# Performance work log

Hardware: AMD Instinct MI355X
Metric: run time of the kernel (lower is better)

The kernel has to match this reference:

```python
import jax, jax.numpy as jnp
import numpy as np
import math

B, T, C, H = 16384, 64, 48, 48


def setup_inputs() -> dict:
    key = jax.random.key(0)
    kx, kq, kk, kv = jax.random.split(key, 4)
    return {
        "x": jax.random.normal(kx, (B, T, C), dtype=jnp.float32),
        "Wq": jax.random.normal(kq, (C, H), dtype=jnp.float32) * 0.02,
        "Wk": jax.random.normal(kk, (C, H), dtype=jnp.float32) * 0.02,
        "Wv": jax.random.normal(kv, (C, H), dtype=jnp.float32) * 0.02,
    }


def reference(x, Wq, Wk, Wv):
    # x: [B, T, C]; projections (Linear with bias=False): [B, T, H]
    q = x @ Wq
    k = x @ Wk
    v = x @ Wv
    scale = 1.0 / math.sqrt(H)
    # scores: [B, T, T]
    wei = jnp.einsum("bth,bsh->bts", q, k) * scale
    causal = jnp.tril(jnp.ones((T, T), dtype=bool))  # tril mask, T==BLOCK_SIZE
    wei = jnp.where(causal, wei, -jnp.inf)
    wei = jax.nn.softmax(wei, axis=-1)
    # dropout is identity in eval mode
    return jnp.einsum("bts,bsh->bth", wei, v)
```

## Files before the change

kernel.cpp:

```cpp
#include <hip/hip_runtime.h>
#include <math.h>

typedef __bf16 bf16x8 __attribute__((ext_vector_type(8)));
typedef float f32x4 __attribute__((ext_vector_type(4)));
typedef unsigned short u16;

__device__ __forceinline__ u16 f2b(float f) {
  unsigned u = __builtin_bit_cast(unsigned, f);
  u = (u + 0x7fffu + ((u >> 16) & 1u)) >> 16;
  return (u16)u;
}

__device__ __forceinline__ f32x4 mfma16(bf16x8 a, bf16x8 b, f32x4 c) {
  return __builtin_amdgcn_mfma_f32_16x16x32_bf16(a, b, c, 0, 0, 0);
}

__device__ __forceinline__ int sw(int r, int c) {
  return (r << 6) + ((((c >> 3) ^ r) & 7) << 3) + (c & 7);
}
__device__ __forceinline__ int swc(int r, int ch) {
  return (r << 6) + (((ch ^ r) & 7) << 3);
}

__global__ __launch_bounds__(256) void head_prep(const float* __restrict__ Wq,
                                                 const float* __restrict__ Wk,
                                                 const float* __restrict__ Wv,
                                                 u16* __restrict__ ws) {
  __shared__ float wq[2304], wk[2304], wv[2304];
  const float scale = 0.14433756729740643f;
  for (int i = threadIdx.x; i < 2304; i += 256) {
    wq[i] = Wq[i];
    wk[i] = Wk[i];
    wv[i] = Wv[i];
  }
  __syncthreads();
  for (int idx = threadIdx.x; idx < 96 * 64; idx += 256) {
    int r = idx >> 6, c = idx & 63;
    float v = 0.f;
    if (c < 48) {
      if (r < 48) {
        float a = 0.f;
        for (int h = 0; h < 48; ++h) a += wq[c * 48 + h] * wk[r * 48 + h];
        v = a * scale;
      } else {
        v = wv[c * 48 + (r - 48)];
      }
    }
    ws[sw(r, c)] = f2b(v);
  }
}

__global__ __launch_bounds__(256, 6) void head_main(const float* __restrict__ x,
                                                    const u16* __restrict__ wimg,
                                                    float* __restrict__ out) {
  __shared__ u16 lds[208 * 64];
  u16* const R0 = lds;
  u16* const X  = lds + 96 * 64;
  u16* const VT = lds + 160 * 64;

  const int tid  = threadIdx.x;
  const int lane = tid & 63;
  const int w    = tid >> 6;
  const int qd   = lane >> 4;
  const int col  = lane & 15;
  const long b   = blockIdx.x;

  {
    const uint4* src = (const uint4*)wimg;
    uint4* dst = (uint4*)lds;
    dst[tid]       = src[tid];
    dst[tid + 256] = src[tid + 256];
    dst[tid + 512] = src[tid + 512];
  }
  {
    const float* xb = x + b * 3072;
#pragma unroll
    for (int it = 0; it < 3; ++it) {
      int flat = tid * 4 + it * 1024;
      float4 v = *(const float4*)(xb + flat);
      int row = flat / 48;
      int c0  = flat % 48;
      ushort4 pk;
      pk.x = f2b(v.x); pk.y = f2b(v.y); pk.z = f2b(v.z); pk.w = f2b(v.w);
      *(ushort4*)(X + sw(row, c0)) = pk;
    }
    int zr = tid >> 2;
    int zq = tid & 3;
    ushort4 z = {0, 0, 0, 0};
    *(ushort4*)(X + swc(zr, 6 + (zq >> 1)) + (zq & 1) * 4) = z;
  }
  __syncthreads();

  f32x4 aq[3];
  {
    const int ar = 16 * w + col;
    const bf16x8 xa0 = *(const bf16x8*)(X + swc(ar, qd));
    const bf16x8 xa1 = *(const bf16x8*)(X + swc(ar, qd + 4));
    const u16* WM = R0;
    const u16* WV = R0 + 48 * 64;
#pragma unroll
    for (int n = 0; n < 3; ++n) {
      const int br = 16 * n + col;
      const int b0 = swc(br, qd);
      const int b1 = swc(br, qd + 4);
      f32x4 av = {0.f, 0.f, 0.f, 0.f};
      av = mfma16(xa0, *(const bf16x8*)(WV + b0), av);
      av = mfma16(xa1, *(const bf16x8*)(WV + b1), av);
      f32x4 a = {0.f, 0.f, 0.f, 0.f};
      a = mfma16(xa0, *(const bf16x8*)(WM + b0), a);
      a = mfma16(xa1, *(const bf16x8*)(WM + b1), a);
      aq[n] = a;
      ushort4 pv;
      pv.x = f2b(av[0]); pv.y = f2b(av[1]); pv.z = f2b(av[2]); pv.w = f2b(av[3]);
      *(ushort4*)(VT + sw(16 * n + col, 16 * w + qd * 4)) = pv;
    }
  }
  __syncthreads();

#pragma unroll
  for (int n = 0; n < 3; ++n)
#pragma unroll
    for (int i = 0; i < 4; ++i)
      R0[sw(16 * w + qd * 4 + i, 16 * n + col)] = f2b(aq[n][i]);
  __threadfence_block();

  float sv[4][4];
  {
    const int ar = 16 * w + col;
    const bf16x8 qa0 = *(const bf16x8*)(R0 + swc(ar, qd));
    const bf16x8 qa1 = *(const bf16x8*)(R0 + swc(ar, qd + 4));
#pragma unroll
    for (int st = 0; st < 4; ++st) {
      const int br = 16 * st + col;
      f32x4 a = {0.f, 0.f, 0.f, 0.f};
      a = mfma16(qa0, *(const bf16x8*)(X + swc(br, qd)), a);
      a = mfma16(qa1, *(const bf16x8*)(X + swc(br, qd + 4)), a);
#pragma unroll
      for (int i = 0; i < 4; ++i) sv[st][i] = a[i];
    }
  }

  float m4[4] = {-INFINITY, -INFINITY, -INFINITY, -INFINITY};
#pragma unroll
  for (int st = 0; st < 4; ++st)
#pragma unroll
    for (int i = 0; i < 4; ++i) {
      int tg = 16 * w + qd * 4 + i;
      int sg = 16 * st + col;
      float v = (sg <= tg) ? sv[st][i] : -INFINITY;
      sv[st][i] = v;
      m4[i] = fmaxf(m4[i], v);
    }
#pragma unroll
  for (int d = 1; d < 16; d <<= 1)
#pragma unroll
    for (int i = 0; i < 4; ++i) m4[i] = fmaxf(m4[i], __shfl_xor(m4[i], d, 64));
  float l4[4] = {0.f, 0.f, 0.f, 0.f};
#pragma unroll
  for (int st = 0; st < 4; ++st)
#pragma unroll
    for (int i = 0; i < 4; ++i) {
      float p = __expf(sv[st][i] - m4[i]);
      sv[st][i] = p;
      l4[i] += p;
    }
#pragma unroll
  for (int d = 1; d < 16; d <<= 1)
#pragma unroll
    for (int i = 0; i < 4; ++i) l4[i] += __shfl_xor(l4[i], d, 64);

  __syncthreads();

#pragma unroll
  for (int st = 0; st < 4; ++st)
#pragma unroll
    for (int i = 0; i < 4; ++i)
      X[sw(16 * w + qd * 4 + i, 16 * st + col)] = f2b(sv[st][i]);
  __threadfence_block();

  f32x4 o0 = {0.f, 0.f, 0.f, 0.f}, o1 = o0, o2 = o0;
  {
    const int pr = 16 * w + col;
#pragma unroll
    for (int kt = 0; kt < 2; ++kt) {
      const int ch = qd + 4 * kt;
      bf16x8 pa = *(const bf16x8*)(X + swc(pr, ch));
      o0 = mfma16(pa, *(const bf16x8*)(VT + swc(0  + col, ch)), o0);
      o1 = mfma16(pa, *(const bf16x8*)(VT + swc(16 + col, ch)), o1);
      o2 = mfma16(pa, *(const bf16x8*)(VT + swc(32 + col, ch)), o2);
    }
  }
  float rl[4];
#pragma unroll
  for (int i = 0; i < 4; ++i) rl[i] = __builtin_amdgcn_rcpf(l4[i]);

  float* ob = out + b * 3072 + (16 * w + qd * 4) * 48 + col;
#pragma unroll
  for (int i = 0; i < 4; ++i) {
    ob[i * 48 +  0] = o0[i] * rl[i];
    ob[i * 48 + 16] = o1[i] * rl[i];
    ob[i * 48 + 32] = o2[i] * rl[i];
  }
}

extern "C" void kernel_launch(void* const* d_in, const int* in_sizes, int n_in,
                              void* d_out, int out_size, void* d_ws, size_t ws_size,
                              hipStream_t stream) {
  const float* x  = (const float*)d_in[0];
  const float* Wq = (const float*)d_in[1];
  const float* Wk = (const float*)d_in[2];
  const float* Wv = (const float*)d_in[3];
  u16* wimg = (u16*)d_ws;
  head_prep<<<1, 256, 0, stream>>>(Wq, Wk, Wv, wimg);
  head_main<<<16384, 256, 0, stream>>>(x, wimg, (float*)d_out);
}
```

Baseline: 343.1 us.

## Read weights from global, transpose score MFMAs, and cut LDS footprint and barriers

The main kernel no longer copies the 24 KB weight image into LDS. It now reads the weight fragments directly from global memory, where they should hit in cache, and stores the weight image unswizzled. The Q and score MFMAs swap their operands, so each lane holds one query row's scores, and each softmax reduction needs only two cross-lane shuffles instead of four. The P tile reuses the Q buffer, which removes one __syncthreads and shrinks LDS from 26 KB to 22 KB, so more blocks can fit per CU. Each wave loads only its own 16 rows of x. The cost is global-latency loads for the weights on every block and an extra shuffle to spread the reciprocals.

```diff
diff --git a/kernel.cpp b/kernel.cpp
--- a/kernel.cpp
+++ b/kernel.cpp
@@ -46,17 +46,17 @@
         v = wv[c * 48 + (r - 48)];
       }
     }
-    ws[sw(r, c)] = f2b(v);
+    ws[idx] = f2b(v);
   }
 }
 
 __global__ __launch_bounds__(256, 6) void head_main(const float* __restrict__ x,
                                                     const u16* __restrict__ wimg,
                                                     float* __restrict__ out) {
-  __shared__ u16 lds[208 * 64];
-  u16* const R0 = lds;
-  u16* const X  = lds + 96 * 64;
-  u16* const VT = lds + 160 * 64;
+  __shared__ u16 lds[176 * 64];
+  u16* const QM = lds;
+  u16* const X  = lds + 64 * 64;
+  u16* const VT = lds + 128 * 64;
 
   const int tid  = threadIdx.x;
   const int lane = tid & 63;
@@ -66,140 +66,118 @@
   const long b   = blockIdx.x;
 
   {
-    const uint4* src = (const uint4*)wimg;
-    uint4* dst = (uint4*)lds;
-    dst[tid]       = src[tid];
-    dst[tid + 256] = src[tid + 256];
-    dst[tid + 512] = src[tid + 512];
-  }
-  {
-    const float* xb = x + b * 3072;
+    const float* xb = x + b * 3072 + w * 768;
 #pragma unroll
     for (int it = 0; it < 3; ++it) {
-      int flat = tid * 4 + it * 1024;
-      float4 v = *(const float4*)(xb + flat);
-      int row = flat / 48;
-      int c0  = flat % 48;
+      int e0 = lane * 4 + it * 256;
+      float4 v = *(const float4*)(xb + e0);
+      int row = 16 * w + e0 / 48;
+      int c0  = e0 % 48;
       ushort4 pk;
       pk.x = f2b(v.x); pk.y = f2b(v.y); pk.z = f2b(v.z); pk.w = f2b(v.w);
       *(ushort4*)(X + sw(row, c0)) = pk;
     }
-    int zr = tid >> 2;
-    int zq = tid & 3;
     ushort4 z = {0, 0, 0, 0};
-    *(ushort4*)(X + swc(zr, 6 + (zq >> 1)) + (zq & 1) * 4) = z;
+    *(ushort4*)(X  + sw(16 * w + col, 48 + 4 * qd)) = z;
+    *(ushort4*)(QM + sw(16 * w + col, 48 + 4 * qd)) = z;
   }
   __syncthreads();
 
-  f32x4 aq[3];
-  {
-    const int ar = 16 * w + col;
-    const bf16x8 xa0 = *(const bf16x8*)(X + swc(ar, qd));
-    const bf16x8 xa1 = *(const bf16x8*)(X + swc(ar, qd + 4));
-    const u16* WM = R0;
-    const u16* WV = R0 + 48 * 64;
-#pragma unroll
-    for (int n = 0; n < 3; ++n) {
-      const int br = 16 * n + col;
-      const int b0 = swc(br, qd);
-      const int b1 = swc(br, qd + 4);
-      f32x4 av = {0.f, 0.f, 0.f, 0.f};
-      av = mfma16(xa0, *(const bf16x8*)(WV + b0), av);
-      av = mfma16(xa1, *(const bf16x8*)(WV + b1), av);
-      f32x4 a = {0.f, 0.f, 0.f, 0.f};
-      a = mfma16(xa0, *(const bf16x8*)(WM + b0), a);
-      a = mfma16(xa1, *(const bf16x8*)(WM + b1), a);
-      aq[n] = a;
-      ushort4 pv;
-      pv.x = f2b(av[0]); pv.y = f2b(av[1]); pv.z = f2b(av[2]); pv.w = f2b(av[3]);
-      *(ushort4*)(VT + sw(16 * n + col, 16 * w + qd * 4)) = pv;
-    }
-  }
-  __syncthreads();
+  const int ar = 16 * w + col;
+  const bf16x8 xa0 = *(const bf16x8*)(X + swc(ar, qd));
+  const bf16x8 xa1 = *(const bf16x8*)(X + swc(ar, qd + 4));
 
 #pragma unroll
-  for (int n = 0; n < 3; ++n)
-#pragma unroll
-    for (int i = 0; i < 4; ++i)
-      R0[sw(16 * w + qd * 4 + i, 16 * n + col)] = f2b(aq[n][i]);
-  __threadfence_block();
+  for (int n = 0; n < 3; ++n) {
+    const u16* mrow = wimg + (16 * n + col) * 64;
+    const u16* vrow = wimg + (48 + 16 * n + col) * 64;
+    bf16x8 m0 = *(const bf16x8*)(mrow + 8 * qd);
+    bf16x8 m1 = *(const bf16x8*)(mrow + 8 * qd + 32);
+    bf16x8 v0 = *(const bf16x8*)(vrow + 8 * qd);
+    bf16x8 v1 = *(const bf16x8*)(vrow + 8 * qd + 32);
+    f32x4 aq = {0.f, 0.f, 0.f, 0.f};
+    aq = mfma16(m0, xa0, aq);
+    aq = mfma16(m1, xa1, aq);
+    ushort4 pq;
+    pq.x = f2b(aq[0]); pq.y = f2b(aq[1]); pq.z = f2b(aq[2]); pq.w = f2b(aq[3]);
+    *(ushort4*)(QM + sw(16 * w + col, 16 * n + 4 * qd)) = pq;
+    f32x4 av = {0.f, 0.f, 0.f, 0.f};
+    av = mfma16(xa0, v0, av);
+    av = mfma16(xa1, v1, av);
+    ushort4 pv;
+    pv.x = f2b(av[0]); pv.y = f2b(av[1]); pv.z = f2b(av[2]); pv.w = f2b(av[3]);
+    *(ushort4*)(VT + sw(16 * n + col, 16 * w + 4 * qd)) = pv;
+  }
+
+  __syncthreads();
 
   float sv[4][4];
   {
-    const int ar = 16 * w + col;
-    const bf16x8 qa0 = *(const bf16x8*)(R0 + swc(ar, qd));
-    const bf16x8 qa1 = *(const bf16x8*)(R0 + swc(ar, qd + 4));
+    const bf16x8 qb0 = *(const bf16x8*)(QM + swc(ar, qd));
+    const bf16x8 qb1 = *(const bf16x8*)(QM + swc(ar, qd + 4));
 #pragma unroll
     for (int st = 0; st < 4; ++st) {
       const int br = 16 * st + col;
       f32x4 a = {0.f, 0.f, 0.f, 0.f};
-      a = mfma16(qa0, *(const bf16x8*)(X + swc(br, qd)), a);
-      a = mfma16(qa1, *(const bf16x8*)(X + swc(br, qd + 4)), a);
+      a = mfma16(*(const bf16x8*)(X + swc(br, qd)), qb0, a);
+      a = mfma16(*(const bf16x8*)(X + swc(br, qd + 4)), qb1, a);
 #pragma unroll
       for (int i = 0; i < 4; ++i) sv[st][i] = a[i];
     }
   }
 
-  float m4[4] = {-INFINITY, -INFINITY, -INFINITY, -INFINITY};
+  const int tg = 16 * w + col;
+  float m = -INFINITY;
 #pragma unroll
   for (int st = 0; st < 4; ++st)
 #pragma unroll
     for (int i = 0; i < 4; ++i) {
-      int tg = 16 * w + qd * 4 + i;
-      int sg = 16 * st + col;
+      int sg = 16 * st + 4 * qd + i;
       float v = (sg <= tg) ? sv[st][i] : -INFINITY;
       sv[st][i] = v;
-      m4[i] = fmaxf(m4[i], v);
+      m = fmaxf(m, v);
     }
-#pragma unroll
-  for (int d = 1; d < 16; d <<= 1)
-#pragma unroll
-    for (int i = 0; i < 4; ++i) m4[i] = fmaxf(m4[i], __shfl_xor(m4[i], d, 64));
-  float l4[4] = {0.f, 0.f, 0.f, 0.f};
+  m = fmaxf(m, __shfl_xor(m, 16, 64));
+  m = fmaxf(m, __shfl_xor(m, 32, 64));
+  float l = 0.f;
 #pragma unroll
   for (int st = 0; st < 4; ++st)
 #pragma unroll
     for (int i = 0; i < 4; ++i) {
-      float p = __expf(sv[st][i] - m4[i]);
+      float p = __expf(sv[st][i] - m);
       sv[st][i] = p;
-      l4[i] += p;
+      l += p;
     }
-#pragma unroll
-  for (int d = 1; d < 16; d <<= 1)
-#pragma unroll
-    for (int i = 0; i < 4; ++i) l4[i] += __shfl_xor(l4[i], d, 64);
-
-  __syncthreads();
+  l += __shfl_xor(l, 16, 64);
+  l += __shfl_xor(l, 32, 64);
+  float rl = __builtin_amdgcn_rcpf(l);
 
 #pragma unroll
-  for (int st = 0; st < 4; ++st)
-#pragma unroll
-    for (int i = 0; i < 4; ++i)
-      X[sw(16 * w + qd * 4 + i, 16 * st + col)] = f2b(sv[st][i]);
+  for (int st = 0; st < 4; ++st) {
+    ushort4 pk;
+    pk.x = f2b(sv[st][0]); pk.y = f2b(sv[st][1]);
+    pk.z = f2b(sv[st][2]); pk.w = f2b(sv[st][3]);
+    *(ushort4*)(QM + sw(16 * w + col, 16 * st + 4 * qd)) = pk;
+  }
   __threadfence_block();
 
   f32x4 o0 = {0.f, 0.f, 0.f, 0.f}, o1 = o0, o2 = o0;
-  {
-    const int pr = 16 * w + col;
 #pragma unroll
-    for (int kt = 0; kt < 2; ++kt) {
-      const int ch = qd + 4 * kt;
-      bf16x8 pa = *(const bf16x8*)(X + swc(pr, ch));
-      o0 = mfma16(pa, *(const bf16x8*)(VT + swc(0  + col, ch)), o0);
-      o1 = mfma16(pa, *(const bf16x8*)(VT + swc(16 + col, ch)), o1);
-      o2 = mfma16(pa, *(const bf16x8*)(VT + swc(32 + col, ch)), o2);
-    }
+  for (int kt = 0; kt < 2; ++kt) {
+    const int ch = qd + 4 * kt;
+    bf16x8 pa = *(const bf16x8*)(QM + swc(ar, ch));
+    o0 = mfma16(pa, *(const bf16x8*)(VT + swc(0  + col, ch)), o0);
+    o1 = mfma16(pa, *(const bf16x8*)(VT + swc(16 + col, ch)), o1);
+    o2 = mfma16(pa, *(const bf16x8*)(VT + swc(32 + col, ch)), o2);
   }
-  float rl[4];
-#pragma unroll
-  for (int i = 0; i < 4; ++i) rl[i] = __builtin_amdgcn_rcpf(l4[i]);
 
-  float* ob = out + b * 3072 + (16 * w + qd * 4) * 48 + col;
+  float* ob = out + b * 3072 + (16 * w + 4 * qd) * 48 + col;
 #pragma unroll
   for (int i = 0; i < 4; ++i) {
-    ob[i * 48 +  0] = o0[i] * rl[i];
-    ob[i * 48 + 16] = o1[i] * rl[i];
-    ob[i * 48 + 32] = o2[i] * rl[i];
+    float rli = __shfl(rl, 4 * qd + i, 64);
+    ob[i * 48 +  0] = o0[i] * rli;
+    ob[i * 48 + 16] = o1[i] * rli;
+    ob[i * 48 + 32] = o2[i] * rli;
   }
 }
 
```

Result: slower. 378.6 us (+10.4%).
